# Optimization experiments

Measured on AMD Instinct MI355X. Metric: run time of the kernel, lower is better.

## Reference

```python
import jax, jax.numpy as jnp
import numpy as np

V, E, M, Q, K_ANS, L = 100000, 300, 256, 64, 1024, 64
T = K_ANS * L
WINDOW_SIZES = (1, 2, 3, 4, 5)


def setup_inputs() -> dict:
    key = jax.random.key(0)
    ks = jax.random.split(key, 16)
    s = 0.05
    inp = {
        "data_q": jax.random.randint(ks[0], (Q,), 0, V, dtype=jnp.int32),
        "data_as_word": jax.random.randint(ks[1], (T,), 0, V, dtype=jnp.int32),
        "sizes": jnp.full((K_ANS,), L, dtype=jnp.int32),
        "emb": jax.random.normal(ks[2], (V, E), jnp.float32) * s,
        "W1": jax.random.normal(ks[3], (E, M), jnp.float32) * s,
        "b1": jnp.zeros((M,), jnp.float32),
        "W2": jax.random.normal(ks[4], (E, M), jnp.float32) * s,
        "b2": jnp.zeros((M,), jnp.float32),
        "Wl": jax.random.normal(ks[5], (len(WINDOW_SIZES) * M, M), jnp.float32) * s,
        "bl": jnp.zeros((M,), jnp.float32),
        "Ws": jax.random.normal(ks[6], (M, 1), jnp.float32) * s,
        "bs": jnp.zeros((1,), jnp.float32),
    }
    for i, w in enumerate(WINDOW_SIZES):
        inp[f"Wc{i+1}"] = jax.random.normal(ks[7 + i], (M, M, w), jnp.float32) * s
        inp[f"bc{i+1}"] = jnp.zeros((M,), jnp.float32)
    return inp


def _dmax(c, sizes, w):
    # Dynamic max pool: c is [Lc, M] conv+relu over the concatenated answer axis;
    # each answer k owns conv positions [start_k, start_k + sizes_k - w + 1).
    starts = jnp.concatenate([jnp.zeros((1,), sizes.dtype), jnp.cumsum(sizes)[:-1]])
    pos = jnp.arange(c.shape[0])
    seg = jnp.searchsorted(starts, pos, side="right") - 1  # answer id per position
    valid = pos < starts[seg] + sizes[seg] - (w - 1)
    vals = jnp.where(valid[:, None], c, -jnp.inf)
    return jax.ops.segment_max(vals, seg, num_segments=sizes.shape[0])  # [K, M]


def reference(data_q, data_as_word, sizes, emb, W1, b1, W2, b2,
              Wc1, bc1, Wc2, bc2, Wc3, bc3, Wc4, bc4, Wc5, bc5, Wl, bl, Ws, bs):
    # Gated projection layer: sigmoid(Wx) * tanh(Wx)
    proj = lambda x: jax.nn.sigmoid(x @ W1 + b1) * jnp.tanh(x @ W2 + b2)
    q_p = proj(emb[data_q])        # [Q, M]
    a_p = proj(emb[data_as_word])  # [T, M]
    # Attention: mm -> softmax over dim 0 of attention.T -> mm (as in original)
    att = q_p @ a_p.T                       # [Q, T]
    w_att = jax.nn.softmax(att.T, axis=0)   # [T, Q]
    ctx = w_att @ q_p                       # [T, M]
    sim = a_p * ctx                         # compare step ('mul')  [T, M]
    # Conv + dynamic max pooling per window size
    x = sim.T[None]                         # [1, M, T]
    convs = ((Wc1, bc1), (Wc2, bc2), (Wc3, bc3), (Wc4, bc4), (Wc5, bc5))
    pools = []
    for wsz, (Wc, bc) in zip(WINDOW_SIZES, convs):
        c = jax.lax.conv_general_dilated(
            x, Wc, (1,), "VALID", dimension_numbers=("NCH", "OIH", "NCH"))[0].T  # [T-w+1, M]
        c = jax.nn.relu(c + bc)
        pools.append(_dmax(c, sizes, wsz))  # [K, M]
    h = jnp.tanh(jnp.concatenate(pools, axis=1) @ Wl + bl)  # [K, M]
    logits = (h @ Ws + bs).reshape(-1)                       # [K]
    return jax.nn.log_softmax(logits, axis=0)
```

## Files before the change

kernel.cpp:

```cpp
#include <hip/hip_runtime.h>

typedef unsigned short u16;
typedef unsigned int u32;
using s16x8 = __attribute__((ext_vector_type(8))) short;
using f32x4 = __attribute__((ext_vector_type(4))) float;
using u16x4 = __attribute__((ext_vector_type(4))) u16;

#define DEV __device__ __forceinline__

DEV u16 f2bf(float f) {
    u32 u = __builtin_bit_cast(u32, f);
    u32 r = (u + 0x7FFFu + ((u >> 16) & 1u)) >> 16;
    return (u16)r;
}
DEV float bf2f(u16 h) { return __builtin_bit_cast(float, ((u32)h) << 16); }

DEV f32x4 mfma16(s16x8 a, s16x8 b, f32x4 c) {
    return __builtin_amdgcn_mfma_f32_16x16x32_bf16(a, b, c, 0, 0, 0);
}

#define GLOAD(g, l) __builtin_amdgcn_global_load_lds( \
    (const __attribute__((address_space(1))) unsigned int*)(g), \
    (__attribute__((address_space(3))) unsigned int*)(l), 16, 0, 0)

__global__ void k_prep(const float* W1, const float* W2, const float* Wl,
                       const float* Wc1, const float* Wc2, const float* Wc3,
                       const float* Wc4, const float* Wc5,
                       u16* WpT, u16* WlT, u16* WcT,
                       const int* sizes, int* starts) {
    int tid = threadIdx.x;
    if (blockIdx.x == 5760) {
        __shared__ int ps[256];
        int t4 = tid * 4;
        int v0 = sizes[t4], v1 = sizes[t4 + 1], v2 = sizes[t4 + 2], v3 = sizes[t4 + 3];
        int sum = v0 + v1 + v2 + v3;
        ps[tid] = sum;
        __syncthreads();
        for (int off = 1; off < 256; off <<= 1) {
            int add = (tid >= off) ? ps[tid - off] : 0;
            __syncthreads();
            ps[tid] += add;
            __syncthreads();
        }
        int base = tid ? ps[tid - 1] : 0;
        starts[t4] = base;
        starts[t4 + 1] = base + v0;
        starts[t4 + 2] = base + v0 + v1;
        starts[t4 + 3] = base + v0 + v1 + v2;
        return;
    }
    int idx = blockIdx.x * 256 + tid;
    if (idx < 512 * 320) {
        int n = idx / 320, k = idx - n * 320;
        float v = 0.f;
        if (k < 300) v = (n < 256) ? W1[k * 256 + n] : W2[k * 256 + (n - 256)];
        WpT[idx] = f2bf(v);
    } else if (idx < 512 * 320 + 256 * 1280) {
        int j2 = idx - 512 * 320;
        int m = j2 / 1280, j = j2 - m * 1280;
        WlT[j2] = f2bf(Wl[j * 256 + m]);
    } else {
        int j3 = idx - (512 * 320 + 256 * 1280);
        if (j3 < 983040) {
            int wsz; int off;
            if (j3 < 65536)       { wsz = 1; off = 0; }
            else if (j3 < 196608) { wsz = 2; off = 65536; }
            else if (j3 < 393216) { wsz = 3; off = 196608; }
            else if (j3 < 655360) { wsz = 4; off = 393216; }
            else                  { wsz = 5; off = 655360; }
            int loc = j3 - off;
            int o = loc / (256 * wsz);
            int kk = loc - o * (256 * wsz);
            int dw = kk >> 8, i = kk & 255;
            const float* W = (wsz == 1) ? Wc1 : (wsz == 2) ? Wc2 : (wsz == 3) ? Wc3
                             : (wsz == 4) ? Wc4 : Wc5;
            WcT[j3] = f2bf(W[(o * 256 + i) * wsz + dw]);
        }
    }
}

__launch_bounds__(512)
__global__ void k_proj(const int* data_as, const int* data_q, const float* emb,
                       const u16* WpT, const float* b1, const float* b2,
                       u16* ap, u16* qp) {
    __shared__ u16 X[64 * 320];
    int tid = threadIdx.x;
    bool isq = (blockIdx.x == 1024);
    const int* idx = isq ? data_q : data_as;
    u16* out = isq ? qp : ap;
    long row0 = isq ? 0 : (long)blockIdx.x * 64;
    {
        int r = tid >> 3, part = tid & 7;
        const float* src = emb + (long)idx[row0 + r] * 300;
        float4 f[10];
#pragma unroll
        for (int i = 0; i < 10; ++i) {
            int c0 = part * 40 + i * 4;
            if (c0 < 300) f[i] = *(const float4*)(src + c0);
            else f[i] = float4{0.f, 0.f, 0.f, 0.f};
        }
        char* xrow = (char*)X + r * 640;
        u32 swz = (u32)((r & 7) << 4);
#pragma unroll
        for (int i = 0; i < 5; ++i) {
            int c0 = part * 40 + i * 8;
            s16x8 h;
            h[0] = (short)f2bf(f[2 * i].x);     h[1] = (short)f2bf(f[2 * i].y);
            h[2] = (short)f2bf(f[2 * i].z);     h[3] = (short)f2bf(f[2 * i].w);
            h[4] = (short)f2bf(f[2 * i + 1].x); h[5] = (short)f2bf(f[2 * i + 1].y);
            h[6] = (short)f2bf(f[2 * i + 1].z); h[7] = (short)f2bf(f[2 * i + 1].w);
            *(s16x8*)(xrow + ((u32)(c0 * 2) ^ swz)) = h;
        }
    }
    __syncthreads();
    int wv = tid >> 6, lane = tid & 63, l15 = lane & 15, lq = lane >> 4;
    f32x4 acc[4][4] = {};
    for (int s = 0; s < 10; ++s) {
        s16x8 a[4], b[4];
#pragma unroll
        for (int c = 0; c < 4; ++c) {
            int mt = 2 * wv + (c & 1) + (c >> 1) * 16;
            int o = mt * 16 + l15;
            a[c] = *(const s16x8*)(WpT + o * 320 + s * 32 + lq * 8);
        }
#pragma unroll
        for (int nt = 0; nt < 4; ++nt) {
            int r = nt * 16 + l15;
            b[nt] = *(const s16x8*)((const char*)X + r * 640 +
                                    ((u32)(s * 64 + lq * 16) ^ ((u32)(r & 7) << 4)));
        }
#pragma unroll
        for (int c = 0; c < 4; ++c)
#pragma unroll
            for (int nt = 0; nt < 4; ++nt)
                acc[c][nt] = mfma16(a[c], b[nt], acc[c][nt]);
    }
    __syncthreads();
    u16* Y = X;
#pragma unroll
    for (int c = 0; c < 2; ++c) {
        int o0 = (2 * wv + c) * 16 + lq * 4;
#pragma unroll
        for (int nt = 0; nt < 4; ++nt) {
            int t = nt * 16 + l15;
            u16x4 h4;
#pragma unroll
            for (int r = 0; r < 4; ++r) {
                float xs = acc[c][nt][r] + b1[o0 + r];
                float xt = acc[c + 2][nt][r] + b2[o0 + r];
                float v = (1.f / (1.f + __expf(-xs))) * tanhf(xt);
                h4[r] = f2bf(v);
            }
            *(u16x4*)((char*)Y + t * 528 + o0 * 2) = h4;
        }
    }
    __syncthreads();
    for (int j = tid; j < 2048; j += 512) {
        int t = j >> 5, c8 = (j & 31) * 8;
        *(s16x8*)(out + (row0 + t) * 256 + c8) =
            *(const s16x8*)((const char*)Y + t * 528 + c8 * 2);
    }
}

__launch_bounds__(256)
__global__ void k_att(const u16* qp, const u16* ap, float* att,
                      float* partm, float* parts) {
    __shared__ u16 Q[64 * 256];
    __shared__ u16 A[64 * 256];
    __shared__ float Pm[8][64], Ps[8][64], Qm[64];
    int tid = threadIdx.x;
    long t0 = (long)blockIdx.x * 64;
    for (int j = tid; j < 2048; j += 256) {
        int r = j >> 5, c8 = (j & 31) * 8;
        u32 dst = (u32)(c8 * 2) ^ ((u32)(r & 7) << 4);
        *(s16x8*)((char*)Q + r * 512 + dst) = *(const s16x8*)(qp + r * 256 + c8);
        *(s16x8*)((char*)A + r * 512 + dst) = *(const s16x8*)(ap + (t0 + r) * 256 + c8);
    }
    __syncthreads();
    int wv = tid >> 6, lane = tid & 63, l15 = lane & 15, lq = lane >> 4;
    f32x4 acc[4] = {};
    for (int s = 0; s < 8; ++s) {
        int brow = wv * 16 + l15;
        s16x8 b = *(const s16x8*)((const char*)A + brow * 512 +
                                  ((u32)(s * 64 + lq * 16) ^ ((u32)(brow & 7) << 4)));
#pragma unroll
        for (int mt = 0; mt < 4; ++mt) {
            int arow = mt * 16 + l15;
            s16x8 a = *(const s16x8*)((const char*)Q + arow * 512 +
                                      ((u32)(s * 64 + lq * 16) ^ ((u32)(arow & 7) << 4)));
            acc[mt] = mfma16(a, b, acc[mt]);
        }
    }
#pragma unroll
    for (int mt = 0; mt < 4; ++mt) {
        long t = t0 + wv * 16 + l15;
        *(f32x4*)(att + t * 64 + mt * 16 + lq * 4) = acc[mt];
    }
    float mxv[16];
#pragma unroll
    for (int mt = 0; mt < 4; ++mt)
#pragma unroll
        for (int r = 0; r < 4; ++r) mxv[mt * 4 + r] = acc[mt][r];
#pragma unroll
    for (int off = 1; off <= 8; off <<= 1)
#pragma unroll
        for (int i = 0; i < 16; ++i)
            mxv[i] = fmaxf(mxv[i], __shfl_xor(mxv[i], off, 64));
    if (l15 == 0) {
#pragma unroll
        for (int mt = 0; mt < 4; ++mt)
#pragma unroll
            for (int r = 0; r < 4; ++r)
                Pm[wv][mt * 16 + lq * 4 + r] = mxv[mt * 4 + r];
    }
    __syncthreads();
    if (tid < 64) {
        float g = Pm[0][tid];
#pragma unroll
        for (int i = 1; i < 8; ++i) g = fmaxf(g, Pm[i][tid]);
        Qm[tid] = g;
    }
    __syncthreads();
    float sv[16];
#pragma unroll
    for (int mt = 0; mt < 4; ++mt)
#pragma unroll
        for (int r = 0; r < 4; ++r) {
            int q = mt * 16 + lq * 4 + r;
            sv[mt * 4 + r] = __expf(acc[mt][r] - Qm[q]);
        }
#pragma unroll
    for (int off = 1; off <= 8; off <<= 1)
#pragma unroll
        for (int i = 0; i < 16; ++i)
            sv[i] += __shfl_xor(sv[i], off, 64);
    if (l15 == 0) {
#pragma unroll
        for (int mt = 0; mt < 4; ++mt)
#pragma unroll
            for (int r = 0; r < 4; ++r)
                Ps[wv][mt * 16 + lq * 4 + r] = sv[mt * 4 + r];
    }
    __syncthreads();
    if (tid < 64) {
        float s = Ps[0][tid];
#pragma unroll
        for (int i = 1; i < 8; ++i) s += Ps[i][tid];
        partm[blockIdx.x * 64 + tid] = Qm[tid];
        parts[blockIdx.x * 64 + tid] = s;
    }
}

__launch_bounds__(512)
__global__ void k_red2(const float* partm, const float* parts, float* mx, float* rden) {
    __shared__ float Lm[8][64], Ls[8][64];
    int q = threadIdx.x & 63, sub = threadIdx.x >> 6;
    float m = -3.0e38f, s = 0.f;
    for (int b = sub; b < 1024; b += 8) {
        float m2 = partm[b * 64 + q], s2 = parts[b * 64 + q];
        float mn = fmaxf(m, m2);
        s = s * __expf(m - mn) + s2 * __expf(m2 - mn);
        m = mn;
    }
    Lm[sub][q] = m; Ls[sub][q] = s;
    __syncthreads();
    if (sub == 0) {
#pragma unroll
        for (int i = 1; i < 8; ++i) {
            float m2 = Lm[i][q], s2 = Ls[i][q];
            float mn = fmaxf(m, m2);
            s = s * __expf(m - mn) + s2 * __expf(m2 - mn);
            m = mn;
        }
        mx[q] = m;
        rden[q] = 1.f / s;
    }
}

__launch_bounds__(256)
__global__ void k_ctx(const float* att, const float* mx, const float* rden,
                      const u16* qp, const u16* ap, u16* sim) {
    __shared__ u16 P[64 * 64];
    __shared__ u16 QT[256 * 64];
    __shared__ u16 Y[64 * 264];
    __shared__ float MX[64], RD[64];
    int tid = threadIdx.x;
    long t0 = (long)blockIdx.x * 64;
    if (tid < 64) { MX[tid] = mx[tid]; RD[tid] = rden[tid]; }
    {
        int m = tid;
        char* row = (char*)QT + m * 128;
        u32 swz = (u32)((m & 7) << 4);
        for (int q = 0; q < 64; ++q)
            *(u16*)(row + ((u32)(q * 2) ^ swz)) = qp[q * 256 + m];
    }
    __syncthreads();
    {
        int t = tid >> 2, qq = tid & 3;
        const float* arow = att + (t0 + t) * 64 + qq * 16;
        char* prow = (char*)P + t * 128;
        u32 swz = (u32)((t & 7) << 4);
#pragma unroll
        for (int i4 = 0; i4 < 4; ++i4) {
            float4 fv = *(const float4*)(arow + i4 * 4);
            int q0 = qq * 16 + i4 * 4;
            float p0 = __expf(fv.x - MX[q0 + 0]) * RD[q0 + 0];
            float p1 = __expf(fv.y - MX[q0 + 1]) * RD[q0 + 1];
            float p2 = __expf(fv.z - MX[q0 + 2]) * RD[q0 + 2];
            float p3 = __expf(fv.w - MX[q0 + 3]) * RD[q0 + 3];
            *(u16*)(prow + ((u32)((q0 + 0) * 2) ^ swz)) = f2bf(p0);
            *(u16*)(prow + ((u32)((q0 + 1) * 2) ^ swz)) = f2bf(p1);
            *(u16*)(prow + ((u32)((q0 + 2) * 2) ^ swz)) = f2bf(p2);
            *(u16*)(prow + ((u32)((q0 + 3) * 2) ^ swz)) = f2bf(p3);
        }
    }
    __syncthreads();
    int wv = tid >> 6, lane = tid & 63, l15 = lane & 15, lq = lane >> 4;
    f32x4 acc[16] = {};
#pragma unroll
    for (int s = 0; s < 2; ++s) {
        int arow = wv * 16 + l15;
        s16x8 a = *(const s16x8*)((const char*)P + arow * 128 +
                                  ((u32)(s * 64 + lq * 16) ^ ((u32)(arow & 7) << 4)));
#pragma unroll
        for (int nt = 0; nt < 16; ++nt) {
            int br = nt * 16 + l15;
            s16x8 b = *(const s16x8*)((const char*)QT + br * 128 +
                                      ((u32)(s * 64 + lq * 16) ^ ((u32)(br & 7) << 4)));
            acc[nt] = mfma16(a, b, acc[nt]);
        }
    }
#pragma unroll
    for (int nt = 0; nt < 16; ++nt) {
        int m = nt * 16 + l15;
        int t = wv * 16 + lq * 4;
#pragma unroll
        for (int r = 0; r < 4; ++r) Y[(t + r) * 264 + m] = f2bf(acc[nt][r]);
    }
    __syncthreads();
    for (int j = tid; j < 2048; j += 256) {
        int t = j >> 5, c8 = (j & 31) * 8;
        s16x8 y = *(const s16x8*)(Y + t * 264 + c8);
        s16x8 a8 = *(const s16x8*)(ap + (t0 + t) * 256 + c8);
        s16x8 o;
#pragma unroll
        for (int e = 0; e < 8; ++e)
            o[e] = (short)f2bf(bf2f((u16)a8[e]) * bf2f((u16)y[e]));
        *(s16x8*)(sim + (t0 + t) * 256 + c8) = o;
    }
}

__launch_bounds__(512)
__global__ void k_conv(const u16* sim, const u16* WcT,
                       const int* starts, const int* sizes,
                       const float* bc1, const float* bc2, const float* bc3,
                       const float* bc4, const float* bc5,
                       u16* pools, int Ttot) {
    __shared__ u16 LB[2][32768];
    int tid = threadIdx.x;
    int wv = tid >> 6, lane = tid & 63, l15 = lane & 15, lq = lane >> 4;
    int wm = wv >> 2, wn = wv & 3;
    int b = blockIdx.x;
    long s0 = starts[4 * b];
    int row8 = lane >> 3, seg = lane & 7;
    u32 sA = ((u32)(seg * 16)) ^ (((u32)(row8 & 7)) << 4);

    auto STAGE = [&](int nb, int w_, int dw_, int ic_) {
        int Krow = 256 * w_;
        long wbase = 65536L * ((w_ * (w_ - 1)) / 2);
#pragma unroll
        for (int it = 0; it < 4; ++it) {
            int c = wv * 4 + it;
            long g = s0 + dw_ + c * 8 + row8;
            if (g >= Ttot) g = Ttot - 1;
            const char* srcA = (const char*)sim + g * 512 + ic_ * 128 + sA;
            GLOAD(srcA, (char*)LB[nb] + c * 1024);
        }
#pragma unroll
        for (int it = 0; it < 4; ++it) {
            int c = wv * 4 + it;
            int o = c * 8 + row8;
            const char* srcB = (const char*)WcT +
                2L * (wbase + (long)o * Krow + dw_ * 256 + ic_ * 64) + sA;
            GLOAD(srcB, (char*)LB[nb] + 32768 + c * 1024);
        }
    };
    auto ADV = [](int& w_, int& dw_, int& ic_) {
        if (++ic_ == 4) { ic_ = 0; if (++dw_ == w_) { dw_ = 0; ++w_; } }
    };

    int wS = 1, dwS = 0, icS = 0;
    STAGE(0, wS, dwS, icS);
    ADV(wS, dwS, icS);
    __syncthreads();

    int buf = 0;
    f32x4 acc[8][4] = {};
    int wC = 1, dwC = 0, icC = 0;
    for (int t = 0; t < 60; ++t) {
        if (t < 59) { STAGE(buf ^ 1, wS, dwS, icS); ADV(wS, dwS, icS); }
        const char* Ab = (const char*)LB[buf];
        const char* Bb = (const char*)LB[buf] + 32768;
#pragma unroll
        for (int ks = 0; ks < 2; ++ks) {
            s16x8 A8[8], B4[4];
#pragma unroll
            for (int mt = 0; mt < 8; ++mt) {
                int row = wm * 128 + mt * 16 + l15;
                A8[mt] = *(const s16x8*)(Ab + row * 128 +
                          (((u32)(ks * 64 + lq * 16)) ^ (((u32)(row & 7)) << 4)));
            }
#pragma unroll
            for (int nt = 0; nt < 4; ++nt) {
                int o = wn * 64 + nt * 16 + l15;
                B4[nt] = *(const s16x8*)(Bb + o * 128 +
                          (((u32)(ks * 64 + lq * 16)) ^ (((u32)(o & 7)) << 4)));
            }
            __builtin_amdgcn_s_setprio(1);
#pragma unroll
            for (int mt = 0; mt < 8; ++mt)
#pragma unroll
                for (int nt = 0; nt < 4; ++nt)
                    acc[mt][nt] = mfma16(A8[mt], B4[nt], acc[mt][nt]);
            __builtin_amdgcn_s_setprio(0);
        }
        if (++icC == 4) {
            icC = 0;
            if (++dwC == wC) {
                dwC = 0;
                const float* bc = (wC == 1) ? bc1 : (wC == 2) ? bc2 : (wC == 3) ? bc3
                                  : (wC == 4) ? bc4 : bc5;
#pragma unroll
                for (int a2 = 0; a2 < 2; ++a2) {
                    int kans = b * 4 + wm * 2 + a2;
                    int valid = sizes[kans] - wC + 1;
#pragma unroll
                    for (int nt = 0; nt < 4; ++nt) {
                        float m = -3.0e38f;
#pragma unroll
                        for (int mth = 0; mth < 4; ++mth) {
                            int mt = a2 * 4 + mth;
#pragma unroll
                            for (int r = 0; r < 4; ++r) {
                                int pp = mth * 16 + lq * 4 + r;
                                float v = (pp < valid) ? acc[mt][nt][r] : -3.0e38f;
                                m = fmaxf(m, v);
                            }
                        }
                        m = fmaxf(m, __shfl_xor(m, 16, 64));
                        m = fmaxf(m, __shfl_xor(m, 32, 64));
                        if (lq == 0) {
                            int o = wn * 64 + nt * 16 + l15;
                            float pool = fmaxf(m + bc[o], 0.f);
                            pools[(long)kans * 1280 + (wC - 1) * 256 + o] = f2bf(pool);
                        }
                    }
                }
#pragma unroll
                for (int mt = 0; mt < 8; ++mt)
#pragma unroll
                    for (int nt = 0; nt < 4; ++nt)
                        acc[mt][nt] = f32x4{0.f, 0.f, 0.f, 0.f};
                ++wC;
            }
        }
        __syncthreads();
        buf ^= 1;
    }
}

__launch_bounds__(256)
__global__ void k_head(const u16* pools, const u16* WlT,
                       const float* bl, const float* Ws, const float* bs,
                       float* logits) {
    int tid = threadIdx.x;
    int k0 = blockIdx.x * 64;
    int wv = tid >> 6, lane = tid & 63, l15 = lane & 15, lq = lane >> 4;
    f32x4 acc[4][4] = {};
    for (int s = 0; s < 40; ++s) {
        s16x8 a[4], b[4];
#pragma unroll
        for (int mt = 0; mt < 4; ++mt) {
            int m = (wv * 4 + mt) * 16 + l15;
            a[mt] = *(const s16x8*)(WlT + (long)m * 1280 + s * 32 + lq * 8);
        }
#pragma unroll
        for (int nt = 0; nt < 4; ++nt) {
            int kk = k0 + nt * 16 + l15;
            b[nt] = *(const s16x8*)(pools + (long)kk * 1280 + s * 32 + lq * 8);
        }
#pragma unroll
        for (int mt = 0; mt < 4; ++mt)
#pragma unroll
            for (int nt = 0; nt < 4; ++nt)
                acc[mt][nt] = mfma16(a[mt], b[nt], acc[mt][nt]);
    }
    __shared__ float PS[4][4][16];
#pragma unroll
    for (int nt = 0; nt < 4; ++nt) {
        float p = 0.f;
#pragma unroll
        for (int mt = 0; mt < 4; ++mt) {
            int m0 = (wv * 4 + mt) * 16 + lq * 4;
#pragma unroll
            for (int r = 0; r < 4; ++r) {
                float h = tanhf(acc[mt][nt][r] + bl[m0 + r]);
                p += h * Ws[m0 + r];
            }
        }
        p += __shfl_xor(p, 16, 64);
        p += __shfl_xor(p, 32, 64);
        if (lq == 0) PS[wv][nt][l15] = p;
    }
    __syncthreads();
    if (tid < 64) {
        int nt = tid >> 4, i = tid & 15;
        float v = PS[0][nt][i] + PS[1][nt][i] + PS[2][nt][i] + PS[3][nt][i] + bs[0];
        logits[k0 + nt * 16 + i] = v;
    }
}

__global__ void k_lsm(const float* logits, float* out) {
    __shared__ float r1[16], r2[16];
    int tid = threadIdx.x;
    float v = logits[tid];
    float m = v;
#pragma unroll
    for (int off = 32; off >= 1; off >>= 1) m = fmaxf(m, __shfl_xor(m, off, 64));
    if ((tid & 63) == 0) r1[tid >> 6] = m;
    __syncthreads();
    if (tid < 16) {
        float t = r1[tid];
#pragma unroll
        for (int off = 8; off >= 1; off >>= 1) t = fmaxf(t, __shfl_xor(t, off, 64));
        r1[tid] = t;
    }
    __syncthreads();
    m = r1[0];
    float e = __expf(v - m);
    float s = e;
#pragma unroll
    for (int off = 32; off >= 1; off >>= 1) s += __shfl_xor(s, off, 64);
    if ((tid & 63) == 0) r2[tid >> 6] = s;
    __syncthreads();
    if (tid < 16) {
        float t = r2[tid];
#pragma unroll
        for (int off = 8; off >= 1; off >>= 1) t += __shfl_xor(t, off, 64);
        r2[tid] = t;
    }
    __syncthreads();
    out[tid] = v - m - logf(r2[0]);
}

extern "C" void kernel_launch(void* const* d_in, const int* in_sizes, int n_in,
                              void* d_out, int out_size, void* d_ws, size_t ws_size,
                              hipStream_t stream) {
    const int*   data_q  = (const int*)d_in[0];
    const int*   data_as = (const int*)d_in[1];
    const int*   sizes   = (const int*)d_in[2];
    const float* emb = (const float*)d_in[3];
    const float* W1  = (const float*)d_in[4];
    const float* b1  = (const float*)d_in[5];
    const float* W2  = (const float*)d_in[6];
    const float* b2  = (const float*)d_in[7];
    const float* Wl  = (const float*)d_in[8];
    const float* bl  = (const float*)d_in[9];
    const float* Ws  = (const float*)d_in[10];
    const float* bs  = (const float*)d_in[11];
    const float* Wc1 = (const float*)d_in[12]; const float* bc1 = (const float*)d_in[13];
    const float* Wc2 = (const float*)d_in[14]; const float* bc2 = (const float*)d_in[15];
    const float* Wc3 = (const float*)d_in[16]; const float* bc3 = (const float*)d_in[17];
    const float* Wc4 = (const float*)d_in[18]; const float* bc4 = (const float*)d_in[19];
    const float* Wc5 = (const float*)d_in[20]; const float* bc5 = (const float*)d_in[21];
    int Ttot = in_sizes[1];

    char* ws = (char*)d_ws;
    u16*   WpT    = (u16*)  (ws + 0);
    u16*   WlT    = (u16*)  (ws + 327680);
    u16*   WcT    = (u16*)  (ws + 983040);
    u16*   qp     = (u16*)  (ws + 2949120);
    u16*   ap     = (u16*)  (ws + 2981888);
    float* att    = (float*)(ws + 36536320);
    float* mx     = (float*)(ws + 53379072);
    float* rden   = (float*)(ws + 53379328);
    u16*   sim    = (u16*)  (ws + 53379584);
    u16*   pools  = (u16*)  (ws + 86934016);
    float* logits = (float*)(ws + 89555456);
    int*   starts = (int*)  (ws + 89559552);
    float* partm  = (float*)pools;
    float* parts  = (float*)((char*)pools + 262144);

    k_prep<<<5761, 256, 0, stream>>>(W1, W2, Wl, Wc1, Wc2, Wc3, Wc4, Wc5,
                                     WpT, WlT, WcT, sizes, starts);
    k_proj<<<1025, 512, 0, stream>>>(data_as, data_q, emb, WpT, b1, b2, ap, qp);
    k_att<<<1024, 256, 0, stream>>>(qp, ap, att, partm, parts);
    k_red2<<<1, 512, 0, stream>>>(partm, parts, mx, rden);
    k_ctx<<<1024, 256, 0, stream>>>(att, mx, rden, qp, ap, sim);
    k_conv<<<256, 512, 0, stream>>>(sim, WcT, starts, sizes, bc1, bc2, bc3, bc4, bc5,
                                    pools, Ttot);
    k_head<<<16, 256, 0, stream>>>(pools, WlT, bl, Ws, bs, logits);
    k_lsm<<<1, 1024, 0, stream>>>(logits, (float*)d_out);
}
```

Measured before the change: 333.1 us.

## Split embedding gather into separate kernel and stage bf16 rows via LDS DMA

Splits the projection kernel in two. A new gather kernel reads the embedding rows, converts them to bf16 and writes a padded [T+64, 320] buffer into workspace, reusing the att region. The projection GEMM then loads its tile with global_load_lds using a matching swizzle. The aim is to give the gather wide parallelism and take the fp32 loads and conversion out of the GEMM kernel, at the cost of an extra kernel launch and an extra global write and read of the bf16 activations.

```diff
diff --git a/kernel.cpp b/kernel.cpp
--- a/kernel.cpp
+++ b/kernel.cpp
@@ -80,40 +80,44 @@
 }
 
 __launch_bounds__(512)
-__global__ void k_proj(const int* data_as, const int* data_q, const float* emb,
-                       const u16* WpT, const float* b1, const float* b2,
-                       u16* ap, u16* qp) {
+__global__ void k_gather(const int* data_as, const int* data_q, const float* emb,
+                         u16* xg, int Ttot) {
+    int j = blockIdx.x * 512 + threadIdx.x;
+    int R = Ttot + 64;
+    int row = j / 80;
+    if (row >= R) return;
+    int slot = j - row * 80;
+    int tok = (row < Ttot) ? data_as[row] : data_q[row - Ttot];
+    u16x4 h = {0, 0, 0, 0};
+    if (slot < 75) {
+        float4 f = *(const float4*)(emb + (long)tok * 300 + slot * 4);
+        h[0] = f2bf(f.x); h[1] = f2bf(f.y); h[2] = f2bf(f.z); h[3] = f2bf(f.w);
+    }
+    *(u16x4*)(xg + (long)row * 320 + slot * 4) = h;
+}
+
+__launch_bounds__(512)
+__global__ void k_pgemm(const u16* xg, const u16* WpT, const float* b1, const float* b2,
+                        u16* ap, u16* qp, int Ttot) {
     __shared__ u16 X[64 * 320];
     int tid = threadIdx.x;
     bool isq = (blockIdx.x == 1024);
-    const int* idx = isq ? data_q : data_as;
     u16* out = isq ? qp : ap;
     long row0 = isq ? 0 : (long)blockIdx.x * 64;
+    long grow0 = isq ? Ttot : row0;
+    int wv = tid >> 6, lane = tid & 63, l15 = lane & 15, lq = lane >> 4;
     {
-        int r = tid >> 3, part = tid & 7;
-        const float* src = emb + (long)idx[row0 + r] * 300;
-        float4 f[10];
-#pragma unroll
-        for (int i = 0; i < 10; ++i) {
-            int c0 = part * 40 + i * 4;
-            if (c0 < 300) f[i] = *(const float4*)(src + c0);
-            else f[i] = float4{0.f, 0.f, 0.f, 0.f};
-        }
-        char* xrow = (char*)X + r * 640;
-        u32 swz = (u32)((r & 7) << 4);
 #pragma unroll
         for (int i = 0; i < 5; ++i) {
-            int c0 = part * 40 + i * 8;
-            s16x8 h;
-            h[0] = (short)f2bf(f[2 * i].x);     h[1] = (short)f2bf(f[2 * i].y);
-            h[2] = (short)f2bf(f[2 * i].z);     h[3] = (short)f2bf(f[2 * i].w);
-            h[4] = (short)f2bf(f[2 * i + 1].x); h[5] = (short)f2bf(f[2 * i + 1].y);
-            h[6] = (short)f2bf(f[2 * i + 1].z); h[7] = (short)f2bf(f[2 * i + 1].w);
-            *(s16x8*)(xrow + ((u32)(c0 * 2) ^ swz)) = h;
-        }
-    }
-    __syncthreads();
-    int wv = tid >> 6, lane = tid & 63, l15 = lane & 15, lq = lane >> 4;
+            int G = wv * 320 + i * 64 + lane;
+            int rr = G / 40;
+            int g = G - rr * 40;
+            int gs = g ^ (rr & 7);
+            const char* src = (const char*)(xg + (grow0 + rr) * 320) + gs * 16;
+            GLOAD(src, (char*)X + wv * 5120 + i * 1024);
+        }
+    }
+    __syncthreads();
     f32x4 acc[4][4] = {};
     for (int s = 0; s < 10; ++s) {
         s16x8 a[4], b[4];
@@ -588,12 +592,17 @@
     u16*   pools  = (u16*)  (ws + 86934016);
     float* logits = (float*)(ws + 89555456);
     int*   starts = (int*)  (ws + 89559552);
+    u16*   xg     = (u16*)  (ws + 36536320);
     float* partm  = (float*)pools;
     float* parts  = (float*)((char*)pools + 262144);
 
+    int Rtot = Ttot + 64;
+    int gblocks = (Rtot * 80 + 511) / 512;
+
     k_prep<<<5761, 256, 0, stream>>>(W1, W2, Wl, Wc1, Wc2, Wc3, Wc4, Wc5,
                                      WpT, WlT, WcT, sizes, starts);
-    k_proj<<<1025, 512, 0, stream>>>(data_as, data_q, emb, WpT, b1, b2, ap, qp);
+    k_gather<<<gblocks, 512, 0, stream>>>(data_as, data_q, emb, xg, Ttot);
+    k_pgemm<<<1025, 512, 0, stream>>>(xg, WpT, b1, b2, ap, qp, Ttot);
     k_att<<<1024, 256, 0, stream>>>(qp, ap, att, partm, parts);
     k_red2<<<1, 512, 0, stream>>>(partm, parts, mx, rden);
     k_ctx<<<1024, 256, 0, stream>>>(att, mx, rden, qp, ap, sim);
```

After: 335.4 us (median of 3 runs). Within noise of the previous version (+0.7%).
